# Optimization experiments

Hardware: AMD Instinct MI355X
Metric: run time of the kernel (lower is better)

Reference implementation:

```python
import jax, jax.numpy as jnp
import numpy as np

B, L, D, H, S, E, FF = 4, 2048, 1024, 16, 512, 8, 4096
DH = D // H  # head dim = 64
EPS = 1e-5


def setup_inputs() -> dict:
    key = jax.random.key(0)
    ks = jax.random.split(key, 12)
    std = 0.02
    return {
        "x": jax.random.normal(ks[0], (B, L, D), jnp.float32),
        "slot_query": jax.random.normal(ks[1], (H, S, DH), jnp.float32) * std,
        "slot_key": jax.random.normal(ks[2], (H, S, DH), jnp.float32) * std,
        "w_dispatch_k": jax.random.normal(ks[3], (D, D), jnp.float32) * std,
        "w_dispatch_v": jax.random.normal(ks[4], (D, D), jnp.float32) * std,
        "w_combine_q": jax.random.normal(ks[5], (D, D), jnp.float32) * std,
        "w_in": jax.random.normal(ks[6], (E, FF, D), jnp.float32) * std,
        "b_in": jnp.zeros((E, FF), jnp.float32),
        "w_out": jax.random.normal(ks[7], (E, D, FF), jnp.float32) * std,
        "b_out": jnp.zeros((E, D), jnp.float32),
        "pre_norm_w": jnp.ones((D,), jnp.float32),
        "pre_norm_b": jnp.zeros((D,), jnp.float32),
    }


def _layer_norm(x, w, b, eps=EPS):
    m = jnp.mean(x, axis=-1, keepdims=True)
    v = jnp.mean(jnp.square(x - m), axis=-1, keepdims=True)
    return (x - m) * jax.lax.rsqrt(v + eps) * w + b


def _sdpa(q, k, v):
    # q: (..., Q, d), k: (..., K, d), v: (..., K, d)
    scale = 1.0 / np.sqrt(q.shape[-1])
    scores = jnp.einsum("...qd,...kd->...qk", q, k) * scale
    p = jax.nn.softmax(scores, axis=-1)
    return jnp.einsum("...qk,...kd->...qd", p, v)


def _split_heads(t):  # (B, N, D) -> (B, H, N, DH)
    b, n, _ = t.shape
    return t.reshape(b, n, H, DH).transpose(0, 2, 1, 3)


def _merge_heads(t):  # (B, H, N, DH) -> (B, N, D)
    b, h, n, d = t.shape
    return t.transpose(0, 2, 1, 3).reshape(b, n, h * d)


def reference(x, slot_query, slot_key, w_dispatch_k, w_dispatch_v, w_combine_q,
              w_in, b_in, w_out, b_out, pre_norm_w, pre_norm_b):
    # pre-norm
    xn = _layer_norm(x, pre_norm_w, pre_norm_b)

    # ---- dispatch: slots attend to tokens ----
    k = _split_heads(xn @ w_dispatch_k.T)        # (B,H,L,DH)
    v = _split_heads(xn @ w_dispatch_v.T)        # (B,H,L,DH)
    y = _sdpa(slot_query[None], k, v)            # (B,H,S,DH)
    y = _merge_heads(y)                          # (B,S,D)

    # ---- experts: batched per-expert MLP with relu^2 activation ----
    y = y.reshape(B, E, S // E, D)
    h = jnp.einsum("besd,efd->besf", y, w_in) + b_in[None, :, None, :]
    h = jnp.square(jax.nn.relu(h))               # relu2
    eo = jnp.einsum("besf,edf->besd", h, w_out) + b_out[None, :, None, :]
    eo = eo.reshape(B, S, D)

    # ---- combine: tokens attend to slots ----
    q = _split_heads(xn @ w_combine_q.T)         # (B,H,L,DH)
    vc = _split_heads(eo)                        # (B,H,S,DH)
    o = _sdpa(q, slot_key[None], vc)             # (B,H,L,DH)
    return _merge_heads(o)                       # (B,L,D)
```

## Files before the change

### kernel.cpp

```cpp
#include <hip/hip_runtime.h>
#include <hip/hip_bf16.h>

#define B_  4
#define L_  2048
#define D_  1024
#define H_  16
#define S_  512
#define E_  8
#define FF_ 4096
#define DH_ 64

typedef _Float16 half8 __attribute__((ext_vector_type(8)));
typedef _Float16 half4v __attribute__((ext_vector_type(4)));
typedef float floatx4 __attribute__((ext_vector_type(4)));
typedef unsigned short u16;

__device__ inline u16 f2h(float v) {
  _Float16 x = (_Float16)v;
  return __builtin_bit_cast(u16, x);
}

__device__ inline void gload_lds16(const void* g, void* l) {
  __builtin_amdgcn_global_load_lds(
      (const __attribute__((address_space(1))) void*)g,
      (__attribute__((address_space(3))) void*)l, 16, 0, 0);
}

__device__ inline int swz(int row, int colh) {
  return row * 64 + (colh ^ ((row & 7) << 3));
}
__device__ inline int swz1(int row, int colh) {
  return row * 64 + ((colh & ~7) ^ ((row & 7) << 3)) + (colh & 7);
}

__global__ __launch_bounds__(256) void ln_f16(const float* __restrict__ x,
    const float* __restrict__ w, const float* __restrict__ bb,
    u16* __restrict__ xn) {
  int row = blockIdx.x;
  int tid = threadIdx.x;
  float4 v = ((const float4*)(x + (long)row * D_))[tid];
  float s = v.x + v.y + v.z + v.w;
  __shared__ float red[4];
  #pragma unroll
  for (int off = 32; off > 0; off >>= 1) s += __shfl_down(s, off);
  int wid = tid >> 6, lane = tid & 63;
  if (lane == 0) red[wid] = s;
  __syncthreads();
  float mean = (red[0] + red[1] + red[2] + red[3]) * (1.0f / D_);
  __syncthreads();
  float dx = v.x - mean, dy = v.y - mean, dz = v.z - mean, dw = v.w - mean;
  float s2 = dx*dx + dy*dy + dz*dz + dw*dw;
  #pragma unroll
  for (int off = 32; off > 0; off >>= 1) s2 += __shfl_down(s2, off);
  if (lane == 0) red[wid] = s2;
  __syncthreads();
  float var = (red[0] + red[1] + red[2] + red[3]) * (1.0f / D_);
  float rstd = rsqrtf(var + 1e-5f);
  float4 wv = ((const float4*)w)[tid];
  float4 bv = ((const float4*)bb)[tid];
  half4v o = { (_Float16)(dx * rstd * wv.x + bv.x),
               (_Float16)(dy * rstd * wv.y + bv.y),
               (_Float16)(dz * rstd * wv.z + bv.z),
               (_Float16)(dw * rstd * wv.w + bv.w) };
  *(half4v*)&xn[(long)row * D_ + tid * 4] = o;
}

__global__ __launch_bounds__(256) void wcvt(const float* __restrict__ w0,
    const float* __restrict__ w1, const float* __restrict__ w2,
    const float* __restrict__ sq, const float* __restrict__ skq,
    u16* __restrict__ dst) {
  long i = ((long)blockIdx.x * 256 + threadIdx.x) * 8;
  const float* src; long off; float sc = 1.0f;
  if (i < 3145728) {
    int wsel = (int)(i >> 20);
    src = (wsel == 0) ? w0 : (wsel == 1) ? w1 : w2;
    off = i & 1048575;
  } else if (i < 3670016) {
    src = sq; off = i - 3145728; sc = 0.125f;
  } else {
    src = skq; off = i - 3670016;
  }
  float4 a = *(const float4*)(src + off);
  float4 b = *(const float4*)(src + off + 4);
  half8 h = { (_Float16)(a.x*sc), (_Float16)(a.y*sc), (_Float16)(a.z*sc), (_Float16)(a.w*sc),
              (_Float16)(b.x*sc), (_Float16)(b.y*sc), (_Float16)(b.z*sc), (_Float16)(b.w*sc) };
  *(half8*)(dst + i) = h;
}

__global__ __launch_bounds__(256) void proj_f16(
    const u16* __restrict__ A, const u16* __restrict__ Wc,
    u16* __restrict__ kh, u16* __restrict__ vT, u16* __restrict__ qh) {
  const int wsel = blockIdx.x >> 3;
  const int n0 = (blockIdx.x & 7) * 128, m0 = blockIdx.y * 128;
  const u16* Bh = Wc + (long)wsel * 1048576;
  const int tid = threadIdx.x, l = tid & 63, w = tid >> 6;
  const int wr = w >> 1, wc = w & 1;
  __shared__ __align__(16) u16 As[2][128 * 32];
  __shared__ __align__(16) u16 Bs[2][128 * 32];
  floatx4 acc[4][4] = {};

  const int ck = (l & 3) ^ ((l >> 3) & 3);
  const long gaA0 = (long)(m0 + w * 32 + (l >> 2)) * D_ + ck * 8;
  const long gaA1 = gaA0 + 16 * D_;
  const long gaB0 = (long)(n0 + w * 32 + (l >> 2)) * D_ + ck * 8;
  const long gaB1 = gaB0 + 16 * D_;

  #define PSTAGE(buf, kt)                                          \
    do {                                                           \
      gload_lds16(A + gaA0 + (kt), &As[buf][(w * 32) * 32]);       \
      gload_lds16(A + gaA1 + (kt), &As[buf][(w * 32 + 16) * 32]);  \
      gload_lds16(Bh + gaB0 + (kt), &Bs[buf][(w * 32) * 32]);      \
      gload_lds16(Bh + gaB1 + (kt), &Bs[buf][(w * 32 + 16) * 32]); \
    } while (0)

  PSTAGE(0, 0);
  __syncthreads();

  int cur = 0;
  const int q = l >> 4;
  for (int t = 0; t < 32; ++t) {
    if (t < 31) PSTAGE(cur ^ 1, (t + 1) * 32);
    half8 af[4], bfr[4];
    #pragma unroll
    for (int fr = 0; fr < 4; ++fr) {
      int row = wr * 64 + fr * 16 + (l & 15);
      af[fr] = *(const half8*)&As[cur][row * 32 + ((q ^ ((row >> 1) & 3)) << 3)];
    }
    #pragma unroll
    for (int fc = 0; fc < 4; ++fc) {
      int rr = wc * 64 + fc * 16 + (l & 15);
      bfr[fc] = *(const half8*)&Bs[cur][rr * 32 + ((q ^ ((rr >> 1) & 3)) << 3)];
    }
    #pragma unroll
    for (int fr = 0; fr < 4; ++fr)
      #pragma unroll
      for (int fc = 0; fc < 4; ++fc)
        acc[fr][fc] = __builtin_amdgcn_mfma_f32_16x16x32_f16(af[fr], bfr[fc], acc[fr][fc], 0, 0, 0);
    __syncthreads();
    cur ^= 1;
  }
  #undef PSTAGE

  if (wsel == 1) {
    #pragma unroll
    for (int fr = 0; fr < 4; ++fr)
      #pragma unroll
      for (int fc = 0; fc < 4; ++fc) {
        int row = m0 + wr * 64 + fr * 16 + (l >> 4) * 4;
        int col = n0 + wc * 64 + fc * 16 + (l & 15);
        half4v o = { (_Float16)acc[fr][fc][0], (_Float16)acc[fr][fc][1],
                     (_Float16)acc[fr][fc][2], (_Float16)acc[fr][fc][3] };
        long idx = ((long)(row >> 11) * 1024 + col) * 2048 + (row & 2047);
        *(half4v*)&vT[idx] = o;
      }
  } else {
    u16* C = (wsel == 0) ? kh : qh;
    const float sc = (wsel == 2) ? 0.125f : 1.0f;
    #pragma unroll
    for (int fr = 0; fr < 4; ++fr)
      #pragma unroll
      for (int fc = 0; fc < 4; ++fc)
        #pragma unroll
        for (int r = 0; r < 4; ++r) {
          int row = m0 + wr * 64 + fr * 16 + (l >> 4) * 4 + r;
          int col = n0 + wc * 64 + fc * 16 + (l & 15);
          C[(long)row * D_ + col] = f2h(acc[fr][fc][r] * sc);
        }
  }
}

template<int MODE>
__global__ __launch_bounds__(512) void expert_gemm(
    const u16* __restrict__ A, const float* __restrict__ Bw,
    const float* __restrict__ bias, u16* __restrict__ Ch,
    float* __restrict__ Cp) {
  constexpr int LDA = (MODE == 1) ? D_ : FF_;
  constexpr int LDB = (MODE == 1) ? D_ : FF_;
  const int e = blockIdx.z;
  const int n0 = blockIdx.x * 64;
  const int kc0 = (MODE == 2) ? blockIdx.y * 1024 : 0;
  const int tid = threadIdx.x, l = tid & 63, w = tid >> 6;
  const int wm = w >> 1, wn = w & 1;
  const int lr = l & 15, q = l >> 4;

  __shared__ __align__(16) u16  As[2][256 * 32];
  __shared__ __align__(16) float Bs[2][64 * 32];

  long asrc[2];
  #pragma unroll
  for (int i = 0; i < 2; ++i) {
    int ar = w * 32 + i * 16 + (l >> 2);
    long grow = (MODE == 1) ? ((long)(ar >> 6) * 512 + e * 64 + (ar & 63))
                            : (((long)(ar >> 6) * 8 + e) * 64 + (ar & 63));
    int ck = (l & 3) ^ (ar & 3);
    asrc[i] = grow * (long)LDA + kc0 + ck * 8;
  }
  const float* Bp = Bw + (long)e * (D_ * FF_);
  int brow = w * 8 + (l >> 3);
  int bck = (l & 7) ^ (brow & 7);
  long bsrc = (long)(n0 + brow) * LDB + kc0 + bck * 4;

  floatx4 acc[4][2] = {};

  #define STAGE(buf, kt)                                                 \
    do {                                                                 \
      gload_lds16(A + asrc[0] + (kt), &As[buf][(w * 32) * 32]);          \
      gload_lds16(A + asrc[1] + (kt), &As[buf][(w * 32 + 16) * 32]);     \
      gload_lds16(Bp + bsrc + (kt), &Bs[buf][(w * 8) * 32]);             \
    } while (0)

  STAGE(0, 0);
  __syncthreads();

  int cur = 0;
  for (int t = 0; t < 32; ++t) {
    if (t < 31) STAGE(cur ^ 1, (t + 1) * 32);
    half8 af[4];
    #pragma unroll
    for (int fr = 0; fr < 4; ++fr) {
      int row = wm * 64 + fr * 16 + lr;
      af[fr] = *(const half8*)&As[cur][row * 32 + ((q ^ (row & 3)) << 3)];
    }
    half8 bf[2];
    #pragma unroll
    for (int fc = 0; fc < 2; ++fc) {
      int rn = wn * 32 + fc * 16 + lr;
      float4 x0 = *(const float4*)&Bs[cur][rn * 32 + (((2 * q) ^ (rn & 7)) << 2)];
      float4 x1 = *(const float4*)&Bs[cur][rn * 32 + (((2 * q + 1) ^ (rn & 7)) << 2)];
      bf[fc] = (half8){ (_Float16)x0.x, (_Float16)x0.y, (_Float16)x0.z, (_Float16)x0.w,
                        (_Float16)x1.x, (_Float16)x1.y, (_Float16)x1.z, (_Float16)x1.w };
    }
    #pragma unroll
    for (int fr = 0; fr < 4; ++fr)
      #pragma unroll
      for (int fc = 0; fc < 2; ++fc)
        acc[fr][fc] = __builtin_amdgcn_mfma_f32_16x16x32_f16(af[fr], bf[fc], acc[fr][fc], 0, 0, 0);
    __syncthreads();
    cur ^= 1;
  }
  #undef STAGE

  #pragma unroll
  for (int fr = 0; fr < 4; ++fr)
    #pragma unroll
    for (int fc = 0; fc < 2; ++fc)
      #pragma unroll
      for (int r = 0; r < 4; ++r) {
        int ar = wm * 64 + fr * 16 + q * 4 + r;
        int col = n0 + wn * 32 + fc * 16 + lr;
        float val = acc[fr][fc][r];
        if constexpr (MODE == 1) {
          val += bias[e * FF_ + col];
          val = fmaxf(val, 0.f);
          val *= val;
          Ch[(((long)(ar >> 6) * 8 + e) * 64 + (ar & 63)) * FF_ + col] = f2h(val);
        } else {
          Cp[(((long)blockIdx.y * 8 + e) * 256 + ar) * 1024 + col] = val;
        }
      }
}

__global__ __launch_bounds__(256) void eo_reduce(const float* __restrict__ pb,
    const float* __restrict__ b_out, u16* __restrict__ eoT) {
  long j4 = (long)blockIdx.x * 256 + threadIdx.x;
  long j = j4 * 4;
  float4 s = ((const float4*)pb)[j4];
  #pragma unroll
  for (int c = 1; c < 4; ++c) {
    float4 t = ((const float4*)(pb + (long)c * 2097152))[j4];
    s.x += t.x; s.y += t.y; s.z += t.z; s.w += t.w;
  }
  int e = (int)(j >> 18);
  int rem = (int)(j & 262143);
  int row = rem >> 10, col = rem & 1023;
  float4 bv = *(const float4*)(b_out + e * 1024 + col);
  s.x += bv.x; s.y += bv.y; s.z += bv.z; s.w += bv.w;
  int b = row >> 6;
  int slot = e * 64 + (row & 63);
  float sv[4] = { s.x, s.y, s.z, s.w };
  #pragma unroll
  for (int i = 0; i < 4; ++i) {
    long idx = ((long)b * 1024 + col + i) * 512 + slot;
    eoT[idx] = f2h(sv[i]);
  }
}

template<bool OF32>
__global__ __launch_bounds__(256) void flash_f16(
    const u16* __restrict__ Qg, long qB, long qH, long qR,
    const u16* __restrict__ Kg, long kB, long kH, long kR,
    const u16* __restrict__ VTg, long vB, long vH, long vR,
    void* __restrict__ Og, long oB, long oH, long oR,
    float* __restrict__ pd, float* __restrict__ pacc,
    int Nq, int Nk, int nC) {
  __shared__ __align__(16) u16 Ks[64 * 64];
  __shared__ __align__(16) u16 Vt[64 * 64];
  __shared__ __align__(16) u16 Ps[4][16 * 64];
  const int tid = threadIdx.x, l = tid & 63, w = tid >> 6;
  const int bh = blockIdx.z, b = bh >> 4, hd = bh & 15;
  const int q0 = blockIdx.x * 64 + w * 16;
  const int chunk = Nk / nC;
  const int k0 = blockIdx.y * chunk;

  half8 qf[2];
  #pragma unroll
  for (int ks = 0; ks < 2; ++ks)
    qf[ks] = *(const half8*)(Qg + b * qB + hd * qH +
                             (long)(q0 + (l & 15)) * qR + ks * 32 + (l >> 4) * 8);

  float lrun[4] = { 0.f, 0.f, 0.f, 0.f };
  floatx4 o[4] = {};

  const int sr = tid & 63, cc = tid >> 6;

  for (int t = 0; t < chunk; t += 64) {
    {
      const u16* ksrc = Kg + b * kB + hd * kH + (long)(k0 + t + sr) * kR + cc * 16;
      *(uint4*)&Ks[swz(sr, cc * 16)]     = *(const uint4*)ksrc;
      *(uint4*)&Ks[swz(sr, cc * 16 + 8)] = *(const uint4*)(ksrc + 8);
    }
    {
      const u16* vsrc = VTg + b * vB + hd * vH + (long)sr * vR + k0 + t + cc * 16;
      *(uint4*)&Vt[swz(sr, cc * 16)]     = *(const uint4*)vsrc;
      *(uint4*)&Vt[swz(sr, cc * 16 + 8)] = *(const uint4*)(vsrc + 8);
    }
    __syncthreads();

    floatx4 s[4];
    #pragma unroll
    for (int j = 0; j < 4; ++j) s[j] = (floatx4){0.f, 0.f, 0.f, 0.f};
    #pragma unroll
    for (int ks = 0; ks < 2; ++ks)
      #pragma unroll
      for (int j = 0; j < 4; ++j) {
        int kr = j * 16 + (l & 15);
        half8 kf = *(const half8*)&Ks[swz(kr, ks * 32 + (l >> 4) * 8)];
        s[j] = __builtin_amdgcn_mfma_f32_16x16x32_f16(qf[ks], kf, s[j], 0, 0, 0);
      }

    #pragma unroll
    for (int r = 0; r < 4; ++r) {
      int qq = (l >> 4) * 4 + r;
      float rs = 0.f;
      #pragma unroll
      for (int j = 0; j < 4; ++j) {
        float p = __expf(s[j][r]);
        rs += p;
        Ps[w][swz1(qq, j * 16 + (l & 15))] = f2h(p);
      }
      lrun[r] += rs;
    }

    #pragma unroll
    for (int ks = 0; ks < 2; ++ks) {
      half8 pa = *(const half8*)&Ps[w][swz(l & 15, ks * 32 + (l >> 4) * 8)];
      #pragma unroll
      for (int n = 0; n < 4; ++n) {
        int dr = n * 16 + (l & 15);
        half8 vf = *(const half8*)&Vt[swz(dr, ks * 32 + (l >> 4) * 8)];
        o[n] = __builtin_amdgcn_mfma_f32_16x16x32_f16(pa, vf, o[n], 0, 0, 0);
      }
    }
    __syncthreads();
  }

  #pragma unroll
  for (int r = 0; r < 4; ++r) {
    lrun[r] += __shfl_xor(lrun[r], 1);
    lrun[r] += __shfl_xor(lrun[r], 2);
    lrun[r] += __shfl_xor(lrun[r], 4);
    lrun[r] += __shfl_xor(lrun[r], 8);
  }

  if (nC == 1) {
    float inv[4];
    #pragma unroll
    for (int r = 0; r < 4; ++r) inv[r] = 1.0f / lrun[r];
    #pragma unroll
    for (int n = 0; n < 4; ++n)
      #pragma unroll
      for (int r = 0; r < 4; ++r) {
        int row = q0 + (l >> 4) * 4 + r;
        int dh = n * 16 + (l & 15);
        float val = o[n][r] * inv[r];
        long off = b * oB + hd * oH + (long)row * oR + dh;
        if (OF32) ((float*)Og)[off] = val;
        else      ((u16*)Og)[off] = f2h(val);
      }
  } else {
    #pragma unroll
    for (int r = 0; r < 4; ++r) {
      int row = q0 + (l >> 4) * 4 + r;
      long idx = ((long)bh * Nq + row) * nC + blockIdx.y;
      if ((l & 15) == 0) pd[idx] = lrun[r];
      #pragma unroll
      for (int n = 0; n < 4; ++n)
        pacc[idx * 64 + n * 16 + (l & 15)] = o[n][r];
    }
  }
}

__global__ __launch_bounds__(256) void finalize_f16(
    const float* __restrict__ pd, const float* __restrict__ pacc,
    u16* __restrict__ outp, int nC, int Nq, long oB, long oH, long oR) {
  int tid = threadIdx.x;
  int row = blockIdx.x * 4 + (tid >> 6);
  int lane = tid & 63;
  long base = (long)row * nC;
  float Dn = 0.f, a = 0.f;
  for (int c = 0; c < nC; ++c) {
    Dn += pd[base + c];
    a += pacc[(base + c) * 64 + lane];
  }
  int bh = row / Nq, qrow = row - bh * Nq;
  int b = bh >> 4, h = bh & 15;
  outp[(long)b * oB + (long)h * oH + (long)qrow * oR + lane] = f2h(a / Dn);
}

extern "C" void kernel_launch(void* const* d_in, const int* in_sizes, int n_in,
                              void* d_out, int out_size, void* d_ws, size_t ws_size,
                              hipStream_t stream) {
  const float* x     = (const float*)d_in[0];
  const float* sq    = (const float*)d_in[1];
  const float* skq   = (const float*)d_in[2];
  const float* wk    = (const float*)d_in[3];
  const float* wv    = (const float*)d_in[4];
  const float* wq    = (const float*)d_in[5];
  const float* w_in  = (const float*)d_in[6];
  const float* b_in  = (const float*)d_in[7];
  const float* w_out = (const float*)d_in[8];
  const float* b_out = (const float*)d_in[9];
  const float* pnw   = (const float*)d_in[10];
  const float* pnb   = (const float*)d_in[11];
  float* out = (float*)d_out;

  u16* ws   = (u16*)d_ws;
  u16* xnh  = ws;
  u16* kh   = xnh + 8388608;
  u16* vTh  = kh  + 8388608;
  u16* qh   = vTh + 8388608;
  u16* yh   = qh  + 8388608;
  u16* hh   = yh  + 2097152;
  u16* eoTh = hh  + 8388608;
  u16* wch  = eoTh + 2097152;
  u16* sqh  = wch + 3145728;
  u16* skh  = wch + 3670016;
  float* pbuf = (float*)(wch + 4194304);
  float* pdb  = pbuf + 8388608;
  float* pacc = pbuf;

  ln_f16<<<8192, 256, 0, stream>>>(x, pnw, pnb, xnh);
  wcvt<<<2048, 256, 0, stream>>>(wk, wv, wq, sq, skq, wch);

  proj_f16<<<dim3(24, 64, 1), 256, 0, stream>>>(xnh, wch, kh, vTh, qh);

  flash_f16<false><<<dim3(8, 4, 64), 256, 0, stream>>>(
      sqh, 0L, (long)(S_ * DH_), (long)DH_,
      kh, (long)(L_ * D_), (long)DH_, (long)D_,
      vTh, (long)(L_ * D_), (long)(DH_ * L_), (long)L_,
      nullptr, 0L, 0L, 0L,
      pdb, pacc, S_, L_, 4);
  finalize_f16<<<8192, 256, 0, stream>>>(pdb, pacc, yh, 4, S_,
      (long)(S_ * D_), (long)DH_, (long)D_);

  expert_gemm<1><<<dim3(64, 1, 8), 512, 0, stream>>>(yh, w_in, b_in, hh, nullptr);
  expert_gemm<2><<<dim3(16, 4, 8), 512, 0, stream>>>(hh, w_out, nullptr, nullptr, pbuf);
  eo_reduce<<<2048, 256, 0, stream>>>(pbuf, b_out, eoTh);

  flash_f16<true><<<dim3(32, 1, 64), 256, 0, stream>>>(
      qh, (long)(L_ * D_), (long)DH_, (long)D_,
      skh, 0L, (long)(S_ * DH_), (long)DH_,
      eoTh, (long)(S_ * D_), (long)(DH_ * S_), (long)S_,
      out, (long)(L_ * D_), (long)DH_, (long)D_,
      nullptr, nullptr, L_, S_, 1);
}
```

Measured before the change: 347.6 us.

## Keep softmax probabilities in registers and load K/V tiles via direct-to-LDS loads

The flash attention kernel now computes S transposed (K as the A operand), so each lane's exp'd scores already form a valid A-fragment for a 16x16x16 MFMA. This removes the per-wave P staging buffer in shared memory along with its write and read round trip. K and V tiles are now loaded with global_load_lds using an XOR swizzled layout, replacing the register-staged copies. The row-sum reduction becomes cross-group shuffles, and the normalizer is redistributed with __shfl, at the cost of using the smaller-K MFMA for the PV product.

```diff
diff --git a/kernel.cpp b/kernel.cpp
--- a/kernel.cpp
+++ b/kernel.cpp
@@ -295,34 +295,34 @@
     int Nq, int Nk, int nC) {
   __shared__ __align__(16) u16 Ks[64 * 64];
   __shared__ __align__(16) u16 Vt[64 * 64];
-  __shared__ __align__(16) u16 Ps[4][16 * 64];
   const int tid = threadIdx.x, l = tid & 63, w = tid >> 6;
+  const int g = l >> 4, lq = l & 15;
   const int bh = blockIdx.z, b = bh >> 4, hd = bh & 15;
   const int q0 = blockIdx.x * 64 + w * 16;
-  const int chunk = Nk / nC;
-  const int k0 = blockIdx.y * chunk;
+  const int chunk = Nk / nC, k0 = blockIdx.y * chunk;
 
   half8 qf[2];
   #pragma unroll
   for (int ks = 0; ks < 2; ++ks)
     qf[ks] = *(const half8*)(Qg + b * qB + hd * qH +
-                             (long)(q0 + (l & 15)) * qR + ks * 32 + (l >> 4) * 8);
-
-  float lrun[4] = { 0.f, 0.f, 0.f, 0.f };
+                             (long)(q0 + lq) * qR + ks * 32 + g * 8);
+
+  const int srow = l >> 3;
+  const int scol = ((l & 7) ^ srow) * 8;
+  const long kbase = b * kB + hd * kH;
+  const long vbase = b * vB + hd * vH;
+
+  float lrun = 0.f;
   floatx4 o[4] = {};
 
-  const int sr = tid & 63, cc = tid >> 6;
-
   for (int t = 0; t < chunk; t += 64) {
-    {
-      const u16* ksrc = Kg + b * kB + hd * kH + (long)(k0 + t + sr) * kR + cc * 16;
-      *(uint4*)&Ks[swz(sr, cc * 16)]     = *(const uint4*)ksrc;
-      *(uint4*)&Ks[swz(sr, cc * 16 + 8)] = *(const uint4*)(ksrc + 8);
-    }
-    {
-      const u16* vsrc = VTg + b * vB + hd * vH + (long)sr * vR + k0 + t + cc * 16;
-      *(uint4*)&Vt[swz(sr, cc * 16)]     = *(const uint4*)vsrc;
-      *(uint4*)&Vt[swz(sr, cc * 16 + 8)] = *(const uint4*)(vsrc + 8);
+    #pragma unroll
+    for (int i = 0; i < 2; ++i) {
+      int u = i * 4 + w;
+      gload_lds16(Kg + kbase + (long)(k0 + t + u * 8 + srow) * kR + scol,
+                  &Ks[u * 8 * 64]);
+      gload_lds16(VTg + vbase + (long)(u * 8 + srow) * vR + k0 + t + scol,
+                  &Vt[u * 8 * 64]);
     }
     __syncthreads();
 
@@ -333,69 +333,60 @@
     for (int ks = 0; ks < 2; ++ks)
       #pragma unroll
       for (int j = 0; j < 4; ++j) {
-        int kr = j * 16 + (l & 15);
-        half8 kf = *(const half8*)&Ks[swz(kr, ks * 32 + (l >> 4) * 8)];
-        s[j] = __builtin_amdgcn_mfma_f32_16x16x32_f16(qf[ks], kf, s[j], 0, 0, 0);
-      }
-
-    #pragma unroll
-    for (int r = 0; r < 4; ++r) {
-      int qq = (l >> 4) * 4 + r;
-      float rs = 0.f;
-      #pragma unroll
-      for (int j = 0; j < 4; ++j) {
+        half8 kf = *(const half8*)&Ks[swz(j * 16 + lq, ks * 32 + g * 8)];
+        s[j] = __builtin_amdgcn_mfma_f32_16x16x32_f16(kf, qf[ks], s[j], 0, 0, 0);
+      }
+
+    half4v pa[4];
+    float rs = 0.f;
+    #pragma unroll
+    for (int j = 0; j < 4; ++j)
+      #pragma unroll
+      for (int r = 0; r < 4; ++r) {
         float p = __expf(s[j][r]);
         rs += p;
-        Ps[w][swz1(qq, j * 16 + (l & 15))] = f2h(p);
-      }
-      lrun[r] += rs;
-    }
-
-    #pragma unroll
-    for (int ks = 0; ks < 2; ++ks) {
-      half8 pa = *(const half8*)&Ps[w][swz(l & 15, ks * 32 + (l >> 4) * 8)];
+        pa[j][r] = (_Float16)p;
+      }
+    lrun += rs;
+
+    #pragma unroll
+    for (int j = 0; j < 4; ++j)
       #pragma unroll
       for (int n = 0; n < 4; ++n) {
-        int dr = n * 16 + (l & 15);
-        half8 vf = *(const half8*)&Vt[swz(dr, ks * 32 + (l >> 4) * 8)];
-        o[n] = __builtin_amdgcn_mfma_f32_16x16x32_f16(pa, vf, o[n], 0, 0, 0);
-      }
-    }
+        half4v vf = *(const half4v*)&Vt[swz1(n * 16 + lq, j * 16 + g * 4)];
+        o[n] = __builtin_amdgcn_mfma_f32_16x16x16f16(pa[j], vf, o[n], 0, 0, 0);
+      }
     __syncthreads();
   }
 
-  #pragma unroll
-  for (int r = 0; r < 4; ++r) {
-    lrun[r] += __shfl_xor(lrun[r], 1);
-    lrun[r] += __shfl_xor(lrun[r], 2);
-    lrun[r] += __shfl_xor(lrun[r], 4);
-    lrun[r] += __shfl_xor(lrun[r], 8);
-  }
+  lrun += __shfl_xor(lrun, 16);
+  lrun += __shfl_xor(lrun, 32);
 
   if (nC == 1) {
-    float inv[4];
-    #pragma unroll
-    for (int r = 0; r < 4; ++r) inv[r] = 1.0f / lrun[r];
+    float inv = 1.0f / lrun;
+    float invr[4];
+    #pragma unroll
+    for (int r = 0; r < 4; ++r) invr[r] = __shfl(inv, g * 4 + r);
     #pragma unroll
     for (int n = 0; n < 4; ++n)
       #pragma unroll
       for (int r = 0; r < 4; ++r) {
-        int row = q0 + (l >> 4) * 4 + r;
-        int dh = n * 16 + (l & 15);
-        float val = o[n][r] * inv[r];
+        int row = q0 + g * 4 + r;
+        int dh = n * 16 + lq;
+        float val = o[n][r] * invr[r];
         long off = b * oB + hd * oH + (long)row * oR + dh;
         if (OF32) ((float*)Og)[off] = val;
         else      ((u16*)Og)[off] = f2h(val);
       }
   } else {
+    if (l < 16) pd[((long)bh * Nq + q0 + l) * nC + blockIdx.y] = lrun;
     #pragma unroll
     for (int r = 0; r < 4; ++r) {
-      int row = q0 + (l >> 4) * 4 + r;
+      int row = q0 + g * 4 + r;
       long idx = ((long)bh * Nq + row) * nC + blockIdx.y;
-      if ((l & 15) == 0) pd[idx] = lrun[r];
       #pragma unroll
       for (int n = 0; n < 4; ++n)
-        pacc[idx * 64 + n * 16 + (l & 15)] = o[n][r];
+        pacc[idx * 64 + n * 16 + lq] = o[n][r];
     }
   }
 }
```

After: 322.8 us. -7.1%, faster.
